# Kernel tuning notes

Hardware: AMD Instinct MI355X
Metric: run time of the kernel (lower is better)

The kernel has to match this reference:

```python
import jax, jax.numpy as jnp
import numpy as np

N = 100000
E = 1600000
F_IN = 128
F_OUT = 128
BN_EPS = 1e-5


def setup_inputs() -> dict:
    key = jax.random.key(0)
    ks = jax.random.split(key, 8)
    x = jax.random.normal(ks[0], (N, F_IN), dtype=jnp.float32)
    edge_index = jax.random.randint(ks[1], (2, E), 0, N, dtype=jnp.int64)
    s1 = 1.0 / np.sqrt(F_IN)
    s2 = 1.0 / np.sqrt(F_OUT)
    W1 = jax.random.uniform(ks[2], (F_OUT, F_IN), jnp.float32, -s1, s1)
    b1 = jax.random.uniform(ks[3], (F_OUT,), jnp.float32, -s1, s1)
    gamma = jnp.ones((F_OUT,), jnp.float32)
    beta = jnp.zeros((F_OUT,), jnp.float32)
    W2 = jax.random.uniform(ks[4], (F_OUT, F_OUT), jnp.float32, -s2, s2)
    b2 = jax.random.uniform(ks[5], (F_OUT,), jnp.float32, -s2, s2)
    eps = jnp.zeros((1,), jnp.float32)
    return {"x": x, "edge_index": edge_index, "eps": eps, "W1": W1, "b1": b1,
            "gamma": gamma, "beta": beta, "W2": W2, "b2": b2}


def reference(x, edge_index, eps, W1, b1, gamma, beta, W2, b2):
    row, col = edge_index[0], edge_index[1]
    # gather neighbor features then scatter-add by destination node
    neighbor_sum = jax.ops.segment_sum(x[col], row, num_segments=x.shape[0])
    out = (1.0 + eps) * x + neighbor_sum  # [N, F_IN]
    h = out @ W1.T + b1                   # [N, F_OUT]
    # BatchNorm1d in training mode: biased batch statistics over nodes
    mean = jnp.mean(h, axis=0)
    var = jnp.mean(jnp.square(h - mean), axis=0)
    h = (h - mean) * jax.lax.rsqrt(var + BN_EPS) * gamma + beta
    h = jax.nn.relu(h)
    return h @ W2.T + b2
```

## Files before the change

kernel.cpp:

```cpp
#include <hip/hip_runtime.h>
#include <hip/hip_bf16.h>

#define NF 128

typedef __attribute__((ext_vector_type(8))) short short8;
typedef __attribute__((ext_vector_type(4))) float f32x4;

__device__ __forceinline__ ushort f2bf(float f) {
    union { __hip_bfloat16 h; ushort u; } c;
    c.h = __float2bfloat16(f);
    return c.u;
}
__device__ __forceinline__ float bf_lo(uint u) { return __uint_as_float(u << 16); }
__device__ __forceinline__ float bf_hi(uint u) { return __uint_as_float(u & 0xffff0000u); }

#define EPB 4096
#define CAP 12800

__global__ void cvtsort_kernel(const float* __restrict__ x, const float* __restrict__ W1,
                               const float* __restrict__ W2, ushort* __restrict__ xb,
                               ushort* __restrict__ W1b, ushort* __restrict__ W2b,
                               const int* __restrict__ ei, int* __restrict__ binOff,
                               uint2* __restrict__ pairS, int nx4, int nblkC, int E) {
    __shared__ uint2 sorted[EPB];
    __shared__ int lcnt[256];
    __shared__ int lofs[256];
    __shared__ int lcur[256];
    __shared__ int gdelta[256];
    int t = threadIdx.x;
    int blk = blockIdx.x;
    if (blk < nblkC) {
        lcnt[t] = 0;
        lcur[t] = 0;
        __syncthreads();
        int base = blk * EPB;
        int rows[EPB / 256], cols[EPB / 256];
#pragma unroll
        for (int it = 0; it < EPB / 256; it++) {
            int e = base + it * 256 + t;
            rows[it] = (e < E) ? ei[e] : -1;
            cols[it] = (e < E) ? ei[E + e] : 0;
            if (rows[it] >= 0) atomicAdd(&lcnt[rows[it] >> 9], 1);
        }
        __syncthreads();
        int v = lcnt[t];
        lofs[t] = v;
        __syncthreads();
#pragma unroll
        for (int off = 1; off < 256; off <<= 1) {
            int u = (t >= off) ? lofs[t - off] : 0;
            __syncthreads();
            lofs[t] += u;
            __syncthreads();
        }
        int myOfs = lofs[t] - v;
        int g = v ? atomicAdd(&binOff[t], v) : 0;
        __syncthreads();
        lofs[t] = myOfs;
        gdelta[t] = t * CAP + g - myOfs;
        __syncthreads();
#pragma unroll
        for (int it = 0; it < EPB / 256; it++) {
            if (rows[it] >= 0) {
                int b = rows[it] >> 9;
                int p = lofs[b] + atomicAdd(&lcur[b], 1);
                sorted[p] = make_uint2((uint)rows[it], (uint)cols[it]);
            }
        }
        __syncthreads();
        int nvalid = min(EPB, E - base);
        for (int i = t; i < nvalid; i += 256) {
            uint2 pr = sorted[i];
            pairS[gdelta[pr.x >> 9] + i] = pr;
        }
    }
    int gid = blk * 256 + t;
    const float* src;
    ushort* dst;
    int idx;
    if (gid < nx4) { src = x; dst = xb; idx = gid; }
    else if (gid < nx4 + 4096) { src = W1; dst = W1b; idx = gid - nx4; }
    else if (gid < nx4 + 8192) { src = W2; dst = W2b; idx = gid - nx4 - 4096; }
    else return;
    float4 v = reinterpret_cast<const float4*>(src)[idx];
    ushort4 o;
    o.x = f2bf(v.x); o.y = f2bf(v.y); o.z = f2bf(v.z); o.w = f2bf(v.w);
    reinterpret_cast<ushort4*>(dst)[idx] = o;
}

__global__ void passDE_kernel(const uint2* __restrict__ pairS, const int* __restrict__ binOff,
                              int* __restrict__ rowptr, int* __restrict__ adj, int N, int E) {
    __shared__ int hist[512];
    __shared__ int s2[256];
    __shared__ int cur[512];
    int t = threadIdx.x;
    int b = blockIdx.x;
    hist[t] = 0;
    hist[t + 256] = 0;
    s2[t] = (t < b) ? binOff[t] : 0;
    __syncthreads();
#pragma unroll
    for (int off = 128; off > 0; off >>= 1) {
        if (t < off) s2[t] += s2[t + off];
        __syncthreads();
    }
    int base = s2[0];
    int cnt = binOff[b];
    size_t pbase = (size_t)b * CAP;
    __syncthreads();
    for (int i = t; i < cnt; i += 256)
        atomicAdd(&hist[pairS[pbase + i].x & 511], 1);
    __syncthreads();
    int h0 = hist[2 * t], h1 = hist[2 * t + 1];
    s2[t] = h0 + h1;
    __syncthreads();
#pragma unroll
    for (int off = 1; off < 256; off <<= 1) {
        int u = (t >= off) ? s2[t - off] : 0;
        __syncthreads();
        s2[t] += u;
        __syncthreads();
    }
    int e0 = base + s2[t] - (h0 + h1);
    int e1 = e0 + h0;
    int g0 = b * 512 + 2 * t;
    if (g0 < N) rowptr[g0] = e0;
    if (g0 + 1 < N) rowptr[g0 + 1] = e1;
    if (t == 0 && b == gridDim.x - 1) rowptr[N] = E;
    cur[2 * t] = e0;
    cur[2 * t + 1] = e1;
    __syncthreads();
    for (int i = t; i < cnt; i += 256) {
        uint2 p = pairS[pbase + i];
        int slot = atomicAdd(&cur[p.x & 511], 1);
        adj[slot] = (int)p.y;
    }
}

#define ACCV(v)                                                   \
    a0 += bf_lo((v).x); a1 += bf_hi((v).x);                       \
    a2 += bf_lo((v).y); a3 += bf_hi((v).y);                       \
    a4 += bf_lo((v).z); a5 += bf_hi((v).z);                       \
    a6 += bf_lo((v).w); a7 += bf_hi((v).w);

__global__ void gather_kernel(const uint4* __restrict__ xb4, const int* __restrict__ rowptr,
                              const int* __restrict__ adj, const float* __restrict__ eps,
                              uint4* __restrict__ aggb4, int N) {
    int t = blockIdx.x * blockDim.x + threadIdx.x;
    int node = t >> 4;
    int lane = t & 15;
    if (node >= N) return;
    uint4 u = xb4[(size_t)node * 16 + lane];
    float s = 1.0f + eps[0];
    float a0 = bf_lo(u.x) * s, a1 = bf_hi(u.x) * s;
    float a2 = bf_lo(u.y) * s, a3 = bf_hi(u.y) * s;
    float a4 = bf_lo(u.z) * s, a5 = bf_hi(u.z) * s;
    float a6 = bf_lo(u.w) * s, a7 = bf_hi(u.w) * s;
    int j = rowptr[node], end = rowptr[node + 1];
    for (; j + 8 <= end; j += 8) {
        int c0 = adj[j],     c1 = adj[j + 1], c2 = adj[j + 2], c3 = adj[j + 3];
        int c4 = adj[j + 4], c5 = adj[j + 5], c6 = adj[j + 6], c7 = adj[j + 7];
        uint4 v0 = xb4[(size_t)c0 * 16 + lane];
        uint4 v1 = xb4[(size_t)c1 * 16 + lane];
        uint4 v2 = xb4[(size_t)c2 * 16 + lane];
        uint4 v3 = xb4[(size_t)c3 * 16 + lane];
        uint4 v4 = xb4[(size_t)c4 * 16 + lane];
        uint4 v5 = xb4[(size_t)c5 * 16 + lane];
        uint4 v6 = xb4[(size_t)c6 * 16 + lane];
        uint4 v7 = xb4[(size_t)c7 * 16 + lane];
        ACCV(v0) ACCV(v1) ACCV(v2) ACCV(v3)
        ACCV(v4) ACCV(v5) ACCV(v6) ACCV(v7)
    }
    if (j + 4 <= end) {
        int c0 = adj[j], c1 = adj[j + 1], c2 = adj[j + 2], c3 = adj[j + 3];
        uint4 v0 = xb4[(size_t)c0 * 16 + lane];
        uint4 v1 = xb4[(size_t)c1 * 16 + lane];
        uint4 v2 = xb4[(size_t)c2 * 16 + lane];
        uint4 v3 = xb4[(size_t)c3 * 16 + lane];
        ACCV(v0) ACCV(v1) ACCV(v2) ACCV(v3)
        j += 4;
    }
    if (j + 2 <= end) {
        int c0 = adj[j], c1 = adj[j + 1];
        uint4 v0 = xb4[(size_t)c0 * 16 + lane];
        uint4 v1 = xb4[(size_t)c1 * 16 + lane];
        ACCV(v0) ACCV(v1)
        j += 2;
    }
    if (j < end) {
        uint4 v0 = xb4[(size_t)adj[j] * 16 + lane];
        ACCV(v0)
    }
    uint4 o;
    o.x = (uint)f2bf(a0) | ((uint)f2bf(a1) << 16);
    o.y = (uint)f2bf(a2) | ((uint)f2bf(a3) << 16);
    o.z = (uint)f2bf(a4) | ((uint)f2bf(a5) << 16);
    o.w = (uint)f2bf(a6) | ((uint)f2bf(a7) << 16);
    aggb4[(size_t)node * 16 + lane] = o;
}

template <int MODE>
__global__ __launch_bounds__(256) void mgemm_kernel(
    const ushort* __restrict__ Ab, const ushort* __restrict__ Wb,
    const float* __restrict__ bias, float* __restrict__ out,
    ushort* __restrict__ hb, float* __restrict__ stats,
    const float* __restrict__ gamma, const float* __restrict__ beta, int N) {
    __shared__ __align__(16) ushort smem[2 * 128 * 136];
    __shared__ float redS[256];
    __shared__ float redQ[256];
    __shared__ float scL[128];
    __shared__ float shL[128];
    ushort* As = smem;
    ushort* Bs = smem + 128 * 136;

    const int t = threadIdx.x;
    const int row0 = blockIdx.x * 128;
    const int r16 = t >> 4;
    const int c8 = (t & 15) * 8;

    if (MODE == 1 && t < 128) {
        float inv_n = 1.0f / (float)N;
        float mean = stats[t] * inv_n;
        float var = fmaxf(stats[128 + t] * inv_n - mean * mean, 0.0f);
        float s = gamma[t] * rsqrtf(var + 1e-5f);
        scL[t] = s;
        shL[t] = beta[t] - mean * s;
    }
    if (MODE == 1) __syncthreads();

    float sc[8], sh[8];
    if (MODE == 1) {
#pragma unroll
        for (int i = 0; i < 8; i++) { sc[i] = scL[c8 + i]; sh[i] = shL[c8 + i]; }
    }

#pragma unroll
    for (int it = 0; it < 8; it++) {
        int row = it * 16 + r16;
        int gr = row0 + row;
        if (MODE == 0) {
            uint4 v = make_uint4(0, 0, 0, 0);
            if (gr < N) v = *reinterpret_cast<const uint4*>(Ab + (size_t)gr * NF + c8);
            *reinterpret_cast<uint4*>(&As[row * 136 + c8]) = v;
        } else {
            uint4 v = make_uint4(0, 0, 0, 0);
            if (gr < N) v = *reinterpret_cast<const uint4*>(hb + (size_t)gr * NF + c8);
            float vv[8] = {bf_lo(v.x), bf_hi(v.x), bf_lo(v.y), bf_hi(v.y),
                           bf_lo(v.z), bf_hi(v.z), bf_lo(v.w), bf_hi(v.w)};
#pragma unroll
            for (int i = 0; i < 8; i++) vv[i] = fmaxf(vv[i] * sc[i] + sh[i], 0.0f);
            uint4 p;
            p.x = (uint)f2bf(vv[0]) | ((uint)f2bf(vv[1]) << 16);
            p.y = (uint)f2bf(vv[2]) | ((uint)f2bf(vv[3]) << 16);
            p.z = (uint)f2bf(vv[4]) | ((uint)f2bf(vv[5]) << 16);
            p.w = (uint)f2bf(vv[6]) | ((uint)f2bf(vv[7]) << 16);
            *reinterpret_cast<uint4*>(&As[row * 136 + c8]) = p;
        }
        uint4 w = *reinterpret_cast<const uint4*>(Wb + row * NF + c8);
        *reinterpret_cast<uint4*>(&Bs[row * 136 + c8]) = w;
    }
    __syncthreads();

    const int wid = t >> 6;
    const int lane = t & 63;
    const int quad = lane >> 4;
    const int l16 = lane & 15;
    const int wm = wid >> 1;
    const int wn = wid & 1;

    f32x4 acc[4][4];
#pragma unroll
    for (int tm = 0; tm < 4; tm++)
#pragma unroll
        for (int tn = 0; tn < 4; tn++) acc[tm][tn] = (f32x4)(0.0f);

#pragma unroll
    for (int ks = 0; ks < 4; ks++) {
        short8 a[4], b[4];
#pragma unroll
        for (int tm = 0; tm < 4; tm++)
            a[tm] = *reinterpret_cast<const short8*>(
                &As[(wm * 64 + tm * 16 + l16) * 136 + ks * 32 + quad * 8]);
#pragma unroll
        for (int tn = 0; tn < 4; tn++)
            b[tn] = *reinterpret_cast<const short8*>(
                &Bs[(wn * 64 + tn * 16 + l16) * 136 + ks * 32 + quad * 8]);
#pragma unroll
        for (int tm = 0; tm < 4; tm++)
#pragma unroll
            for (int tn = 0; tn < 4; tn++)
                acc[tm][tn] = __builtin_amdgcn_mfma_f32_16x16x32_bf16(a[tm], b[tn],
                                                                      acc[tm][tn], 0, 0, 0);
    }

    float bs[4];
#pragma unroll
    for (int tn = 0; tn < 4; tn++) bs[tn] = bias[wn * 64 + tn * 16 + l16];

    __syncthreads();
    ushort* htile = As;
    float* ftile = reinterpret_cast<float*>(smem);

    float ssum[4] = {0.f, 0.f, 0.f, 0.f}, sq[4] = {0.f, 0.f, 0.f, 0.f};
#pragma unroll
    for (int tm = 0; tm < 4; tm++) {
        int rb = wm * 64 + tm * 16 + quad * 4;
#pragma unroll
        for (int reg = 0; reg < 4; reg++) {
            int gr = row0 + rb + reg;
            bool ok = gr < N;
#pragma unroll
            for (int tn = 0; tn < 4; tn++) {
                int col = wn * 64 + tn * 16 + l16;
                float h = acc[tm][tn][reg] + bs[tn];
                if (MODE == 0) {
                    htile[(rb + reg) * 128 + col] = f2bf(h);
                    if (ok) { ssum[tn] += h; sq[tn] += h * h; }
                } else {
                    ftile[(rb + reg) * 128 + col] = h;
                }
            }
        }
    }
    __syncthreads();

    if (MODE == 0) {
        for (int i = t; i < 2048; i += 256) {
            int row = i >> 4;
            int gr = row0 + row;
            if (gr < N)
                *reinterpret_cast<uint4*>(hb + (size_t)gr * NF + (i & 15) * 8) =
                    *reinterpret_cast<const uint4*>(htile + row * 128 + (i & 15) * 8);
        }
    } else {
        for (int i = t; i < 4096; i += 256) {
            int row = i >> 5;
            int gr = row0 + row;
            if (gr < N)
                *reinterpret_cast<float4*>(out + (size_t)gr * NF + (i & 31) * 4) =
                    *reinterpret_cast<const float4*>(ftile + row * 128 + (i & 31) * 4);
        }
    }

    if (MODE == 0) {
#pragma unroll
        for (int tn = 0; tn < 4; tn++) {
            float s = ssum[tn], q = sq[tn];
            s += __shfl_xor(s, 16); s += __shfl_xor(s, 32);
            q += __shfl_xor(q, 16); q += __shfl_xor(q, 32);
            if (quad == 0) {
                int c = wn * 64 + tn * 16 + l16;
                redS[wm * 128 + c] = s;
                redQ[wm * 128 + c] = q;
            }
        }
        __syncthreads();
        if (t < 128) {
            unsafeAtomicAdd(&stats[t], redS[t] + redS[128 + t]);
            unsafeAtomicAdd(&stats[128 + t], redQ[t] + redQ[128 + t]);
        }
    }
}

extern "C" void kernel_launch(void* const* d_in, const int* in_sizes, int n_in,
                              void* d_out, int out_size, void* d_ws, size_t ws_size,
                              hipStream_t stream) {
    const float* x     = (const float*)d_in[0];
    const int* ei      = (const int*)d_in[1];
    const float* eps   = (const float*)d_in[2];
    const float* W1    = (const float*)d_in[3];
    const float* b1    = (const float*)d_in[4];
    const float* gamma = (const float*)d_in[5];
    const float* beta  = (const float*)d_in[6];
    const float* W2    = (const float*)d_in[7];
    const float* b2    = (const float*)d_in[8];
    float* out         = (float*)d_out;

    const int N = in_sizes[0] / NF;
    const int E = in_sizes[1] / 2;

    const int NB = (N + 511) >> 9;
    const int nblkC = (E + EPB - 1) / EPB;

    ushort* xb     = (ushort*)d_ws;
    ushort* aggb   = xb + (size_t)N * NF;
    ushort* W1b    = aggb + (size_t)N * NF;
    ushort* W2b    = W1b + NF * NF;
    float*  stats  = (float*)(W2b + NF * NF);
    int*    binOff = (int*)(stats + 512);
    int*    rowptr = binOff + 256;
    int*    adj    = rowptr + (N + 1);
    uint2*  pairS  = (uint2*)aggb;
    ushort* hb     = xb;

    (void)hipMemsetAsync(stats, 0, 3072, stream);

    int nx4 = N * 32;
    int cvtBlocks = (nx4 + 8192 + 255) / 256;
    cvtsort_kernel<<<cvtBlocks, 256, 0, stream>>>(x, W1, W2, xb, W1b, W2b, ei, binOff,
                                                  pairS, nx4, nblkC, E);
    passDE_kernel<<<NB, 256, 0, stream>>>(pairS, binOff, rowptr, adj, N, E);

    long long gt = (long long)N * 16;
    gather_kernel<<<(int)((gt + 255) / 256), 256, 0, stream>>>((const uint4*)xb, rowptr, adj,
                                                               eps, (uint4*)aggb, N);

    int gblocks = (N + 127) / 128;
    mgemm_kernel<0><<<gblocks, 256, 0, stream>>>(aggb, W1b, b1, out, hb, stats,
                                                 nullptr, nullptr, N);
    mgemm_kernel<1><<<gblocks, 256, 0, stream>>>(nullptr, W2b, b2, out, hb, stats,
                                                 gamma, beta, N);
}
```

Before: 257.2 us.

## Fuse neighbor gather-aggregation into first GEMM kernel's shared-memory tile load

The separate gather kernel is removed. The first GEMM kernel now computes the (1+eps)*x plus neighbor-sum rows directly into its shared-memory A tile, so the bf16 aggregate is no longer written to and read back from global memory, and one launch goes away. Because hb no longer aliases xb, the workspace layout changes: hb gets its own buffer and pairS reuses it. The cost is that the GEMM kernel's occupancy is limited by its large shared-memory footprint, which may reduce the latency hiding available to the irregular gather loads.

```diff
diff --git a/kernel.cpp b/kernel.cpp
--- a/kernel.cpp
+++ b/kernel.cpp
@@ -143,67 +143,12 @@
     a4 += bf_lo((v).z); a5 += bf_hi((v).z);                       \
     a6 += bf_lo((v).w); a7 += bf_hi((v).w);
 
-__global__ void gather_kernel(const uint4* __restrict__ xb4, const int* __restrict__ rowptr,
-                              const int* __restrict__ adj, const float* __restrict__ eps,
-                              uint4* __restrict__ aggb4, int N) {
-    int t = blockIdx.x * blockDim.x + threadIdx.x;
-    int node = t >> 4;
-    int lane = t & 15;
-    if (node >= N) return;
-    uint4 u = xb4[(size_t)node * 16 + lane];
-    float s = 1.0f + eps[0];
-    float a0 = bf_lo(u.x) * s, a1 = bf_hi(u.x) * s;
-    float a2 = bf_lo(u.y) * s, a3 = bf_hi(u.y) * s;
-    float a4 = bf_lo(u.z) * s, a5 = bf_hi(u.z) * s;
-    float a6 = bf_lo(u.w) * s, a7 = bf_hi(u.w) * s;
-    int j = rowptr[node], end = rowptr[node + 1];
-    for (; j + 8 <= end; j += 8) {
-        int c0 = adj[j],     c1 = adj[j + 1], c2 = adj[j + 2], c3 = adj[j + 3];
-        int c4 = adj[j + 4], c5 = adj[j + 5], c6 = adj[j + 6], c7 = adj[j + 7];
-        uint4 v0 = xb4[(size_t)c0 * 16 + lane];
-        uint4 v1 = xb4[(size_t)c1 * 16 + lane];
-        uint4 v2 = xb4[(size_t)c2 * 16 + lane];
-        uint4 v3 = xb4[(size_t)c3 * 16 + lane];
-        uint4 v4 = xb4[(size_t)c4 * 16 + lane];
-        uint4 v5 = xb4[(size_t)c5 * 16 + lane];
-        uint4 v6 = xb4[(size_t)c6 * 16 + lane];
-        uint4 v7 = xb4[(size_t)c7 * 16 + lane];
-        ACCV(v0) ACCV(v1) ACCV(v2) ACCV(v3)
-        ACCV(v4) ACCV(v5) ACCV(v6) ACCV(v7)
-    }
-    if (j + 4 <= end) {
-        int c0 = adj[j], c1 = adj[j + 1], c2 = adj[j + 2], c3 = adj[j + 3];
-        uint4 v0 = xb4[(size_t)c0 * 16 + lane];
-        uint4 v1 = xb4[(size_t)c1 * 16 + lane];
-        uint4 v2 = xb4[(size_t)c2 * 16 + lane];
-        uint4 v3 = xb4[(size_t)c3 * 16 + lane];
-        ACCV(v0) ACCV(v1) ACCV(v2) ACCV(v3)
-        j += 4;
-    }
-    if (j + 2 <= end) {
-        int c0 = adj[j], c1 = adj[j + 1];
-        uint4 v0 = xb4[(size_t)c0 * 16 + lane];
-        uint4 v1 = xb4[(size_t)c1 * 16 + lane];
-        ACCV(v0) ACCV(v1)
-        j += 2;
-    }
-    if (j < end) {
-        uint4 v0 = xb4[(size_t)adj[j] * 16 + lane];
-        ACCV(v0)
-    }
-    uint4 o;
-    o.x = (uint)f2bf(a0) | ((uint)f2bf(a1) << 16);
-    o.y = (uint)f2bf(a2) | ((uint)f2bf(a3) << 16);
-    o.z = (uint)f2bf(a4) | ((uint)f2bf(a5) << 16);
-    o.w = (uint)f2bf(a6) | ((uint)f2bf(a7) << 16);
-    aggb4[(size_t)node * 16 + lane] = o;
-}
-
 template <int MODE>
 __global__ __launch_bounds__(256) void mgemm_kernel(
-    const ushort* __restrict__ Ab, const ushort* __restrict__ Wb,
-    const float* __restrict__ bias, float* __restrict__ out,
-    ushort* __restrict__ hb, float* __restrict__ stats,
+    const uint4* __restrict__ xb4, const int* __restrict__ rowptr,
+    const int* __restrict__ adj, const float* __restrict__ eps,
+    const ushort* __restrict__ Wb, const float* __restrict__ bias,
+    float* __restrict__ out, ushort* __restrict__ hb, float* __restrict__ stats,
     const float* __restrict__ gamma, const float* __restrict__ beta, int N) {
     __shared__ __align__(16) ushort smem[2 * 128 * 136];
     __shared__ float redS[256];
@@ -217,6 +162,7 @@
     const int row0 = blockIdx.x * 128;
     const int r16 = t >> 4;
     const int c8 = (t & 15) * 8;
+    const int lg = t & 15;
 
     if (MODE == 1 && t < 128) {
         float inv_n = 1.0f / (float)N;
@@ -228,21 +174,77 @@
     }
     if (MODE == 1) __syncthreads();
 
-    float sc[8], sh[8];
-    if (MODE == 1) {
+    if (MODE == 0) {
+        float es = 1.0f + eps[0];
+#pragma unroll 1
+        for (int sub = 0; sub < 8; sub++) {
+            int row = sub * 16 + r16;
+            int gr = row0 + row;
+            float a0 = 0.f, a1 = 0.f, a2 = 0.f, a3 = 0.f;
+            float a4 = 0.f, a5 = 0.f, a6 = 0.f, a7 = 0.f;
+            if (gr < N) {
+                uint4 u = xb4[(size_t)gr * 16 + lg];
+                a0 = bf_lo(u.x) * es; a1 = bf_hi(u.x) * es;
+                a2 = bf_lo(u.y) * es; a3 = bf_hi(u.y) * es;
+                a4 = bf_lo(u.z) * es; a5 = bf_hi(u.z) * es;
+                a6 = bf_lo(u.w) * es; a7 = bf_hi(u.w) * es;
+                int j = rowptr[gr], end = rowptr[gr + 1];
+                for (; j + 8 <= end; j += 8) {
+                    int c0 = adj[j],     c1 = adj[j + 1], c2 = adj[j + 2], c3 = adj[j + 3];
+                    int c4 = adj[j + 4], c5 = adj[j + 5], c6 = adj[j + 6], c7 = adj[j + 7];
+                    uint4 v0 = xb4[(size_t)c0 * 16 + lg];
+                    uint4 v1 = xb4[(size_t)c1 * 16 + lg];
+                    uint4 v2 = xb4[(size_t)c2 * 16 + lg];
+                    uint4 v3 = xb4[(size_t)c3 * 16 + lg];
+                    uint4 v4 = xb4[(size_t)c4 * 16 + lg];
+                    uint4 v5 = xb4[(size_t)c5 * 16 + lg];
+                    uint4 v6 = xb4[(size_t)c6 * 16 + lg];
+                    uint4 v7 = xb4[(size_t)c7 * 16 + lg];
+                    ACCV(v0) ACCV(v1) ACCV(v2) ACCV(v3)
+                    ACCV(v4) ACCV(v5) ACCV(v6) ACCV(v7)
+                }
+                if (j + 4 <= end) {
+                    int c0 = adj[j], c1 = adj[j + 1], c2 = adj[j + 2], c3 = adj[j + 3];
+                    uint4 v0 = xb4[(size_t)c0 * 16 + lg];
+                    uint4 v1 = xb4[(size_t)c1 * 16 + lg];
+                    uint4 v2 = xb4[(size_t)c2 * 16 + lg];
+                    uint4 v3 = xb4[(size_t)c3 * 16 + lg];
+                    ACCV(v0) ACCV(v1) ACCV(v2) ACCV(v3)
+                    j += 4;
+                }
+                if (j + 2 <= end) {
+                    int c0 = adj[j], c1 = adj[j + 1];
+                    uint4 v0 = xb4[(size_t)c0 * 16 + lg];
+                    uint4 v1 = xb4[(size_t)c1 * 16 + lg];
+                    ACCV(v0) ACCV(v1)
+                    j += 2;
+                }
+                if (j < end) {
+                    uint4 v0 = xb4[(size_t)adj[j] * 16 + lg];
+                    ACCV(v0)
+                }
+            }
+            uint4 o;
+            o.x = (uint)f2bf(a0) | ((uint)f2bf(a1) << 16);
+            o.y = (uint)f2bf(a2) | ((uint)f2bf(a3) << 16);
+            o.z = (uint)f2bf(a4) | ((uint)f2bf(a5) << 16);
+            o.w = (uint)f2bf(a6) | ((uint)f2bf(a7) << 16);
+            *reinterpret_cast<uint4*>(&As[row * 136 + c8]) = o;
+        }
+#pragma unroll
+        for (int it = 0; it < 8; it++) {
+            int row = it * 16 + r16;
+            uint4 w = *reinterpret_cast<const uint4*>(Wb + row * NF + c8);
+            *reinterpret_cast<uint4*>(&Bs[row * 136 + c8]) = w;
+        }
+    } else {
+        float sc[8], sh[8];
 #pragma unroll
         for (int i = 0; i < 8; i++) { sc[i] = scL[c8 + i]; sh[i] = shL[c8 + i]; }
-    }
-
-#pragma unroll
-    for (int it = 0; it < 8; it++) {
-        int row = it * 16 + r16;
-        int gr = row0 + row;
-        if (MODE == 0) {
-            uint4 v = make_uint4(0, 0, 0, 0);
-            if (gr < N) v = *reinterpret_cast<const uint4*>(Ab + (size_t)gr * NF + c8);
-            *reinterpret_cast<uint4*>(&As[row * 136 + c8]) = v;
-        } else {
+#pragma unroll
+        for (int it = 0; it < 8; it++) {
+            int row = it * 16 + r16;
+            int gr = row0 + row;
             uint4 v = make_uint4(0, 0, 0, 0);
             if (gr < N) v = *reinterpret_cast<const uint4*>(hb + (size_t)gr * NF + c8);
             float vv[8] = {bf_lo(v.x), bf_hi(v.x), bf_lo(v.y), bf_hi(v.y),
@@ -255,9 +257,9 @@
             p.z = (uint)f2bf(vv[4]) | ((uint)f2bf(vv[5]) << 16);
             p.w = (uint)f2bf(vv[6]) | ((uint)f2bf(vv[7]) << 16);
             *reinterpret_cast<uint4*>(&As[row * 136 + c8]) = p;
-        }
-        uint4 w = *reinterpret_cast<const uint4*>(Wb + row * NF + c8);
-        *reinterpret_cast<uint4*>(&Bs[row * 136 + c8]) = w;
+            uint4 w = *reinterpret_cast<const uint4*>(Wb + row * NF + c8);
+            *reinterpret_cast<uint4*>(&Bs[row * 136 + c8]) = w;
+        }
     }
     __syncthreads();
 
@@ -383,15 +385,14 @@
     const int nblkC = (E + EPB - 1) / EPB;
 
     ushort* xb     = (ushort*)d_ws;
-    ushort* aggb   = xb + (size_t)N * NF;
-    ushort* W1b    = aggb + (size_t)N * NF;
+    ushort* hb     = xb + (size_t)N * NF;
+    ushort* W1b    = hb + (size_t)N * NF;
     ushort* W2b    = W1b + NF * NF;
     float*  stats  = (float*)(W2b + NF * NF);
     int*    binOff = (int*)(stats + 512);
     int*    rowptr = binOff + 256;
     int*    adj    = rowptr + (N + 1);
-    uint2*  pairS  = (uint2*)aggb;
-    ushort* hb     = xb;
+    uint2*  pairS  = (uint2*)hb;
 
     (void)hipMemsetAsync(stats, 0, 3072, stream);
 
@@ -401,13 +402,11 @@
                                                   pairS, nx4, nblkC, E);
     passDE_kernel<<<NB, 256, 0, stream>>>(pairS, binOff, rowptr, adj, N, E);
 
-    long long gt = (long long)N * 16;
-    gather_kernel<<<(int)((gt + 255) / 256), 256, 0, stream>>>((const uint4*)xb, rowptr, adj,
-                                                               eps, (uint4*)aggb, N);
-
     int gblocks = (N + 127) / 128;
-    mgemm_kernel<0><<<gblocks, 256, 0, stream>>>(aggb, W1b, b1, out, hb, stats,
+    mgemm_kernel<0><<<gblocks, 256, 0, stream>>>((const uint4*)xb, rowptr, adj, eps,
+                                                 W1b, b1, out, hb, stats,
                                                  nullptr, nullptr, N);
-    mgemm_kernel<1><<<gblocks, 256, 0, stream>>>(nullptr, W2b, b2, out, hb, stats,
+    mgemm_kernel<1><<<gblocks, 256, 0, stream>>>(nullptr, nullptr, nullptr, nullptr,
+                                                 W2b, b2, out, hb, stats,
                                                  gamma, beta, N);
 }
```

After: 262.3 us. Within noise of the previous version (+2.0%).
